# Performance work log

Hardware: AMD Instinct MI355X
Metric: run time of the kernel (lower is better)

## Reference

```python
import jax, jax.numpy as jnp
import numpy as np

N = 50000        # nodes
E = 500000       # edges
NUM = 4          # sampled intermediate neighbors per edge (self.num)
F = 64           # in_feats == out_feats (transform=False)
D = 32           # dist_dim
NB = 64          # embedding rows = len(boundaries)+1


def setup_inputs() -> dict:
    key = jax.random.key(0)
    ks = jax.random.split(key, 10)
    feat = jax.random.normal(ks[0], (N, F), jnp.float32)
    loc = jax.random.uniform(ks[1], (N, 3), jnp.float32)          # 3D positions in unit cube
    boundaries = jnp.sort(jax.random.uniform(ks[2], (NB - 1,), jnp.float32, 0.0, 2.0))
    embed_table = jax.random.normal(ks[3], (NB, D), jnp.float32)
    G_w = jax.random.normal(ks[4], (F, D), jnp.float32) / np.sqrt(D)      # Linear(dist_dim->out, no bias)
    agg_w = jax.random.normal(ks[5], (F, 2 * F), jnp.float32) / np.sqrt(2 * F)  # Linear(2*out->out)
    agg_b = jnp.zeros((F,), jnp.float32)
    src = jax.random.randint(ks[6], (E,), 0, N, jnp.int32)
    dst = jax.random.randint(ks[7], (E,), 0, N, jnp.int32)
    inter_ids = jax.random.randint(ks[8], (E, NUM), 0, N, jnp.int32)
    return dict(feat=feat, loc=loc, boundaries=boundaries, embed_table=embed_table,
                G_w=G_w, agg_w=agg_w, agg_b=agg_b, src=src, dst=dst, inter_ids=inter_ids)


def reference(feat, loc, boundaries, embed_table, G_w, agg_w, agg_b, src, dst, inter_ids):
    n = feat.shape[0]
    ones = jnp.ones((src.shape[0],), feat.dtype)
    # symmetric-ish degree normalization: d0 = in_deg^-0.5, d2 = out_deg^-0.5
    in_deg = jax.ops.segment_sum(ones, dst, num_segments=n)
    out_deg = jax.ops.segment_sum(ones, src, num_segments=n)
    d0 = jnp.clip(in_deg, 1.0) ** -0.5   # [N]
    d2 = jnp.clip(out_deg, 1.0) ** -0.5  # [N]

    # dist1 = ||loc[dst] - loc[src]||_2, bucketize -> embed -> G
    dist1 = jnp.linalg.norm(loc[dst] - loc[src], axis=1)              # [E]
    de1 = embed_table[jnp.searchsorted(boundaries, dist1)] @ G_w.T    # [E, F]

    # intermediate sampled neighbors: dist to each sampled node from edge src
    pos_src = loc[src]                                                # [E, 3]
    inter_pos = loc[inter_ids]                                        # [E, NUM, 3]
    dist_ = jnp.linalg.norm(pos_src[:, None, :] - inter_pos, axis=-1) # [E, NUM]
    de_ = embed_table[jnp.searchsorted(boundaries, dist_)] @ G_w.T    # [E, NUM, F]
    inter_h = feat[inter_ids]                                         # [E, NUM, F]
    dist_embed_dot_h = (de_ * inter_h).mean(axis=1)                   # [E, F]

    # h = d0[dst] * d2[src] * agg_fc([de1 * h_src, dist_embed_dot_h])
    cat = jnp.concatenate([de1 * feat[src], dist_embed_dot_h], axis=1)  # [E, 2F]
    msg = (d0[dst] * d2[src])[:, None] * (cat @ agg_w.T + agg_b)        # [E, F]

    # update_all(copy_e('h'), sum) -> scatter-sum messages to dst
    ft = jax.ops.segment_sum(msg, dst, num_segments=n)                  # [N, F]
    return ft
```

## Files before the change

### kernel.cpp

```cpp
#include <hip/hip_runtime.h>
#include <math.h>

#define LUTN 1024
#define LUTSCALE 512.0f
#define NBINS 50048
#define CHSH 12


__global__ __launch_bounds__(512) void front_kernel(
    const float* __restrict__ embed, const float* __restrict__ G_w,
    const float* __restrict__ boundaries, const float* __restrict__ feat,
    const float* __restrict__ loc,
    const int* __restrict__ src, const int* __restrict__ dst,
    float* __restrict__ M, int* __restrict__ lut,
    unsigned short* __restrict__ featH, float4* __restrict__ loc4,
    unsigned char* __restrict__ pcnt, unsigned char* __restrict__ psrc,
    unsigned char* __restrict__ rnk8,
    int N, int E, int P, int PREPB) {

    __shared__ unsigned int h[NBINS / 4];

    if (blockIdx.x < 2 * P) {
        for (int i = threadIdx.x; i < NBINS / 4; i += 512) h[i] = 0u;
        __syncthreads();

        const int p    = blockIdx.x >> 1;
        const int role = blockIdx.x & 1;
        const int base = p << CHSH;
        const int lim  = min(E - base, 1 << CHSH);

        if (role == 0) {
            for (int t = threadIdx.x; t < lim; t += 512) {
                const int e = base + t;
                const int d = dst[e];
                const unsigned sh = (unsigned)(d & 3) * 8u;
                unsigned old = atomicAdd(&h[d >> 2], 1u << sh);
                rnk8[e] = (unsigned char)((old >> sh) & 0xFFu);
            }
            __syncthreads();
            unsigned int* gc = (unsigned int*)(pcnt + (size_t)p * NBINS);
            for (int i = threadIdx.x; i < NBINS / 4; i += 512) gc[i] = h[i];
        } else {
            for (int t = threadIdx.x; t < lim; t += 512) {
                const int s = src[base + t];
                atomicAdd(&h[s >> 2], 1u << ((unsigned)(s & 3) * 8u));
            }
            __syncthreads();
            unsigned int* gs = (unsigned int*)(psrc + (size_t)p * NBINS);
            for (int i = threadIdx.x; i < NBINS / 4; i += 512) gs[i] = h[i];
        }
        return;
    }

    const int gid = (blockIdx.x - 2 * P) * 512 + threadIdx.x;
    const int gsz = PREPB * 512;
    for (int i = gid; i < 4096; i += gsz) {
        int b = i >> 6, f = i & 63;
        float acc = 0.f;
        #pragma unroll
        for (int dd = 0; dd < 32; ++dd) acc += embed[b * 32 + dd] * G_w[f * 32 + dd];
        M[i] = acc;
    }
    for (int i = gid; i < LUTN; i += gsz) {
        float left = (float)i * (1.0f / LUTSCALE);
        int c = 0;
        for (int j = 0; j < 63; ++j) c += (boundaries[j] < left) ? 1 : 0;
        lut[i] = c;
    }
    const int nq = N * 16;
    for (int i = gid; i < nq; i += gsz) {
        float4 v = ((const float4*)feat)[i];
        unsigned ux = __float_as_uint(v.x), uy = __float_as_uint(v.y);
        unsigned uz = __float_as_uint(v.z), uw = __float_as_uint(v.w);
        ushort4 hh;
        hh.x = (unsigned short)((ux + 0x7FFFu + ((ux >> 16) & 1u)) >> 16);
        hh.y = (unsigned short)((uy + 0x7FFFu + ((uy >> 16) & 1u)) >> 16);
        hh.z = (unsigned short)((uz + 0x7FFFu + ((uz >> 16) & 1u)) >> 16);
        hh.w = (unsigned short)((uw + 0x7FFFu + ((uw >> 16) & 1u)) >> 16);
        ((ushort4*)featH)[i] = hh;
    }
    for (int i = gid; i < N; i += gsz)
        loc4[i] = make_float4(loc[3 * i], loc[3 * i + 1], loc[3 * i + 2], 0.f);
}


__global__ __launch_bounds__(1024) void merge_scan_kernel(
    unsigned char* __restrict__ pcnt, const unsigned char* __restrict__ psrc,
    int* __restrict__ cnt, float* __restrict__ d2w,
    int* __restrict__ startv, int* __restrict__ part, int P, int N) {

    __shared__ int wsum[16];
    const int t = threadIdx.x, lane = t & 63, wv = t >> 6;
    const int d = blockIdx.x * 1024 + t;

    int sc = 0;
    if (d < N) {
        #pragma unroll 4
        for (int p = 0; p < P; ++p) {
            const size_t idx = (size_t)p * NBINS + d;
            const int c = pcnt[idx];
            pcnt[idx] = (unsigned char)sc;
            sc += c;
        }
        cnt[d] = sc;
        int ss = 0;
        #pragma unroll 4
        for (int p = 0; p < P; ++p) ss += psrc[(size_t)p * NBINS + d];
        d2w[d] = rsqrtf(fmaxf((float)ss, 1.0f));
    }

    const int v = sc;
    int x = v;
    #pragma unroll
    for (int off = 1; off < 64; off <<= 1) { int y = __shfl_up(x, off); if (lane >= off) x += y; }
    if (lane == 63) wsum[wv] = x;
    __syncthreads();
    if (t < 16) {
        int w = wsum[t], xx = w;
        #pragma unroll
        for (int off = 1; off < 16; off <<= 1) { int y = __shfl_up(xx, off); if (t >= off) xx += y; }
        wsum[t] = xx - w;
    }
    __syncthreads();
    int incl = x + wsum[wv];
    if (d < N) startv[d] = incl - v;
    if (t == 1023) part[blockIdx.x] = incl;
}

__device__ __forceinline__ void load_chunkoff(const int* __restrict__ part, int nb,
                                              int* __restrict__ co) {
    if (threadIdx.x < 64) {
        int v = (threadIdx.x < nb) ? part[threadIdx.x] : 0;
        int x = v;
        #pragma unroll
        for (int off = 1; off < 64; off <<= 1) {
            int y = __shfl_up(x, off);
            if ((threadIdx.x & 63) >= off) x += y;
        }
        co[threadIdx.x] = x - v;
    }
    __syncthreads();
}


__global__ __launch_bounds__(256) void edge_kernel(
    const float4* __restrict__ loc4, const float* __restrict__ boundaries,
    const int* __restrict__ lut,
    const int* __restrict__ src, const int* __restrict__ dst,
    const int* __restrict__ inter,
    const unsigned char* __restrict__ rnk8, const unsigned char* __restrict__ pcnt,
    const int* __restrict__ startv, const int* __restrict__ part,
    const float* __restrict__ d2w,
    int4* __restrict__ rec, int E, int nb) {

    __shared__ int lut_s[LUTN];
    __shared__ float bl[64];
    __shared__ int co[64];
    ((int4*)lut_s)[threadIdx.x] = ((const int4*)lut)[threadIdx.x];
    if (threadIdx.x < 64)
        bl[threadIdx.x] = (threadIdx.x < 63) ? boundaries[threadIdx.x] : 3.4e38f;
    load_chunkoff(part, nb, co);

    const int ebase = blockIdx.x * 512 + threadIdx.x;

    #pragma unroll
    for (int u = 0; u < 2; ++u) {
        const int e = ebase + u * 256;
        if (e >= E) continue;

        const int s = src[e], d = dst[e];
        const int4 ii = ((const int4*)inter)[e];

        const float4 ps = loc4[s];
        float dist[5];
        {
            float4 pd = loc4[d];
            float dx = pd.x - ps.x, dy = pd.y - ps.y, dz = pd.z - ps.z;
            dist[0] = sqrtf(dx * dx + dy * dy + dz * dz);
        }
        const int id4[4] = {ii.x, ii.y, ii.z, ii.w};
        #pragma unroll
        for (int j = 0; j < 4; ++j) {
            float4 pt = loc4[id4[j]];
            float dx = pt.x - ps.x, dy = pt.y - ps.y, dz = pt.z - ps.z;
            dist[1 + j] = sqrtf(dx * dx + dy * dy + dz * dz);
        }
        unsigned pack = 0;
        #pragma unroll
        for (int q = 0; q < 5; ++q) {
            float dq = dist[q];
            int cell = (int)(dq * LUTSCALE);
            cell = (cell > LUTN - 1) ? (LUTN - 1) : cell;
            int b = lut_s[cell];
            while (b < 63 && bl[b] < dq) ++b;
            while (b > 0 && bl[b - 1] >= dq) --b;
            pack |= ((unsigned)b) << (6 * q);
        }

        const int p = e >> CHSH;
        const int cbase = pcnt[(size_t)p * NBINS + d];
        const int pos = startv[d] + co[d >> 10] + cbase + (int)rnk8[e];
        const float w = d2w[s];
        unsigned uw = __float_as_uint(w);
        unsigned wb = (uw + 0x7FFFu + ((uw >> 16) & 1u)) & 0xFFFF0000u;
        rec[pos] = make_int4(s | (ii.x << 16), ii.y | (ii.z << 16), ii.w | (int)wb, (int)pack);
    }
}


__global__ __launch_bounds__(256) void node_kernel(
    const unsigned short* __restrict__ featH, const float* __restrict__ M,
    const int* __restrict__ cnt, const int* __restrict__ startv,
    const int* __restrict__ part, const int4* __restrict__ rec,
    float* __restrict__ cat, float* __restrict__ swb, int N, int nb) {

    __shared__ float Ms[4096];
    __shared__ int co[64];
    #pragma unroll
    for (int i = 0; i < 4; ++i)
        ((float4*)Ms)[threadIdx.x + 256 * i] = ((const float4*)M)[threadIdx.x + 256 * i];
    load_chunkoff(part, nb, co);

    const int lane = threadIdx.x & 63;
    const int wid  = threadIdx.x >> 6;
    const int d    = blockIdx.x * 4 + wid;
    if (d >= N) return;

    const int deg  = __builtin_amdgcn_readfirstlane(cnt[d]);
    const int base = __builtin_amdgcn_readfirstlane(startv[d] + co[d >> 10]);
    const int4* rp = rec + base;

    float acc0 = 0.f, acc1 = 0.f, sw = 0.f;

    #pragma unroll 4
    for (int k = 0; k < deg; ++k) {
        const int4 r = rp[k];
        const int s  = r.x & 0xFFFF;
        const int i0 = ((unsigned)r.x) >> 16;
        const int i1 = r.y & 0xFFFF;
        const int i2 = ((unsigned)r.y) >> 16;
        const int i3 = r.z & 0xFFFF;
        const float w = __uint_as_float((unsigned)r.z & 0xFFFF0000u);
        const unsigned pk = (unsigned)r.w;

        const float fs = __uint_as_float(((unsigned)featH[(size_t)s  * 64 + lane]) << 16);
        const float f0 = __uint_as_float(((unsigned)featH[(size_t)i0 * 64 + lane]) << 16);
        const float f1 = __uint_as_float(((unsigned)featH[(size_t)i1 * 64 + lane]) << 16);
        const float f2 = __uint_as_float(((unsigned)featH[(size_t)i2 * 64 + lane]) << 16);
        const float f3 = __uint_as_float(((unsigned)featH[(size_t)i3 * 64 + lane]) << 16);
        const float m0 = Ms[(pk & 63u) * 64 + lane];
        const float m1 = Ms[((pk >> 6) & 63u) * 64 + lane];
        const float m2 = Ms[((pk >> 12) & 63u) * 64 + lane];
        const float m3 = Ms[((pk >> 18) & 63u) * 64 + lane];
        const float m4 = Ms[((pk >> 24) & 63u) * 64 + lane];

        acc0 = fmaf(m0 * fs, w, acc0);
        float t = m1 * f0 + m2 * f1 + m3 * f2 + m4 * f3;
        acc1 = fmaf(0.25f * t, w, acc1);
        sw += w;
    }

    cat[(size_t)d * 128 + lane]      = acc0;
    cat[(size_t)d * 128 + 64 + lane] = acc1;
    if (lane == 0) swb[d] = sw;
}


__global__ __launch_bounds__(256) void epilogue_kernel(
    const float* __restrict__ cat, const float* __restrict__ agg_w,
    const float* __restrict__ agg_b, const float* __restrict__ swb,
    const int* __restrict__ cnt, float* __restrict__ out, int N) {

    const int lane = threadIdx.x & 63;
    const int wid  = threadIdx.x >> 6;

    float4 aw[32];
    const float4* awp = (const float4*)(agg_w + (size_t)lane * 128);
    #pragma unroll
    for (int i = 0; i < 32; ++i) aw[i] = awp[i];
    const float bias = agg_b[lane];

    const int gw = blockIdx.x * 4 + wid;
    const int stride = gridDim.x * 4;

    for (int d0i = gw; d0i < N; d0i += stride) {
        const int du = __builtin_amdgcn_readfirstlane(d0i);
        const float* cp = cat + (size_t)du * 128;
        float a0 = bias * swb[du], a1 = 0.f, a2 = 0.f, a3 = 0.f;
        #pragma unroll
        for (int k4 = 0; k4 < 32; k4 += 4) {
            float4 c0 = ((const float4*)cp)[k4];
            float4 c1 = ((const float4*)cp)[k4 + 1];
            float4 c2 = ((const float4*)cp)[k4 + 2];
            float4 c3 = ((const float4*)cp)[k4 + 3];
            a0 = fmaf(aw[k4].x, c0.x, a0); a0 = fmaf(aw[k4].y, c0.y, a0);
            a0 = fmaf(aw[k4].z, c0.z, a0); a0 = fmaf(aw[k4].w, c0.w, a0);
            a1 = fmaf(aw[k4+1].x, c1.x, a1); a1 = fmaf(aw[k4+1].y, c1.y, a1);
            a1 = fmaf(aw[k4+1].z, c1.z, a1); a1 = fmaf(aw[k4+1].w, c1.w, a1);
            a2 = fmaf(aw[k4+2].x, c2.x, a2); a2 = fmaf(aw[k4+2].y, c2.y, a2);
            a2 = fmaf(aw[k4+2].z, c2.z, a2); a2 = fmaf(aw[k4+2].w, c2.w, a2);
            a3 = fmaf(aw[k4+3].x, c3.x, a3); a3 = fmaf(aw[k4+3].y, c3.y, a3);
            a3 = fmaf(aw[k4+3].z, c3.z, a3); a3 = fmaf(aw[k4+3].w, c3.w, a3);
        }
        const float d0v = rsqrtf(fmaxf((float)cnt[du], 1.0f));
        out[(size_t)du * 64 + lane] = d0v * ((a0 + a1) + (a2 + a3));
    }
}


extern "C" void kernel_launch(void* const* d_in, const int* in_sizes, int n_in,
                              void* d_out, int out_size, void* d_ws, size_t ws_size,
                              hipStream_t stream) {
    const float* feat       = (const float*)d_in[0];
    const float* loc        = (const float*)d_in[1];
    const float* boundaries = (const float*)d_in[2];
    const float* embed      = (const float*)d_in[3];
    const float* G_w        = (const float*)d_in[4];
    const float* agg_w      = (const float*)d_in[5];
    const float* agg_b      = (const float*)d_in[6];
    const int*   src        = (const int*)d_in[7];
    const int*   dst        = (const int*)d_in[8];
    const int*   inter      = (const int*)d_in[9];

    const int N = in_sizes[0] / 64;
    const int E = in_sizes[7];

    const int P = (E + (1 << CHSH) - 1) >> CHSH;

    char* w = (char*)d_ws;
    auto take = [&](size_t bytes) { char* p = w; w += (bytes + 15) & ~(size_t)15; return p; };
    float*          M      = (float*)take(4096 * 4);
    int*            lut    = (int*)  take(LUTN * 4);
    int*            cnt    = (int*)  take((size_t)N * 4);
    int*            startv = (int*)  take((size_t)N * 4);
    int*            part   = (int*)  take(64 * 4);
    float*          d2w    = (float*)take((size_t)N * 4);
    int4*           rec    = (int4*) take((size_t)E * 16);
    unsigned char*  rnk8   = (unsigned char*)take((size_t)E);
    unsigned char*  pcnt   = (unsigned char*)take((size_t)P * NBINS);
    unsigned char*  psrc   = (unsigned char*)take((size_t)P * NBINS);
    float*          cat    = (float*)take((size_t)N * 128 * 4);
    float*          swb    = (float*)take((size_t)N * 4);
    unsigned short* featH  = (unsigned short*)take((size_t)N * 64 * 2);
    float4*         loc4   = (float4*)take((size_t)N * 16);
    float*          out    = (float*)d_out;

    const int eb2 = (E + 511) / 512;
    const int nb  = (N + 1023) / 1024;
    const int PREPB = 256;

    front_kernel<<<2 * P + PREPB, 512, 0, stream>>>(embed, G_w, boundaries, feat, loc,
                                                    src, dst, M, lut, featH, loc4,
                                                    pcnt, psrc, rnk8, N, E, P, PREPB);
    merge_scan_kernel<<<nb, 1024, 0, stream>>>(pcnt, psrc, cnt, d2w, startv, part, P, N);
    edge_kernel<<<eb2, 256, 0, stream>>>(loc4, boundaries, lut, src, dst, inter,
                                         rnk8, pcnt, startv, part, d2w, rec, E, nb);
    node_kernel<<<(N + 3) / 4, 256, 0, stream>>>(featH, M, cnt, startv, part, rec,
                                                 cat, swb, N, nb);
    epilogue_kernel<<<768, 256, 0, stream>>>(cat, agg_w, agg_b, swb, cnt, out, N);
}
```

Before: 225.5 us.

## Move per-edge distance bucketing into histogram kernel to overlap with counting

Splits the constant-table and loc4 preparation into a separate small kernel. Per-edge distance computation and bucketization now run in extra blocks of the histogram kernel, concurrently with the degree counting. The later edge kernel becomes a pure scatter that reads a precomputed record and adds the out-degree weight. The aim is to hide the gather-heavy distance work behind the atomic histogram phase. The cost is an extra kernel launch and an additional E×16-byte intermediate write and read.

Result: slower. 237.0 us (+5.1%).

```diff
diff --git a/kernel.cpp b/kernel.cpp
--- a/kernel.cpp
+++ b/kernel.cpp
@@ -7,16 +7,41 @@
 #define CHSH 12
 
 
-__global__ __launch_bounds__(512) void front_kernel(
+__global__ __launch_bounds__(256) void prep0_kernel(
     const float* __restrict__ embed, const float* __restrict__ G_w,
-    const float* __restrict__ boundaries, const float* __restrict__ feat,
-    const float* __restrict__ loc,
+    const float* __restrict__ boundaries, const float* __restrict__ loc,
+    float* __restrict__ M, int* __restrict__ lut,
+    float4* __restrict__ loc4, int N) {
+
+    const int gid = blockIdx.x * 256 + threadIdx.x;
+    const int gsz = gridDim.x * 256;
+    for (int i = gid; i < 4096; i += gsz) {
+        int b = i >> 6, f = i & 63;
+        float acc = 0.f;
+        #pragma unroll
+        for (int dd = 0; dd < 32; ++dd) acc += embed[b * 32 + dd] * G_w[f * 32 + dd];
+        M[i] = acc;
+    }
+    for (int i = gid; i < LUTN; i += gsz) {
+        float left = (float)i * (1.0f / LUTSCALE);
+        int c = 0;
+        for (int j = 0; j < 63; ++j) c += (boundaries[j] < left) ? 1 : 0;
+        lut[i] = c;
+    }
+    for (int i = gid; i < N; i += gsz)
+        loc4[i] = make_float4(loc[3 * i], loc[3 * i + 1], loc[3 * i + 2], 0.f);
+}
+
+
+__global__ __launch_bounds__(512) void front2_kernel(
+    const float* __restrict__ feat, const float4* __restrict__ loc4,
+    const float* __restrict__ boundaries, const int* __restrict__ lut,
     const int* __restrict__ src, const int* __restrict__ dst,
-    float* __restrict__ M, int* __restrict__ lut,
-    unsigned short* __restrict__ featH, float4* __restrict__ loc4,
+    const int* __restrict__ inter,
+    unsigned short* __restrict__ featH,
     unsigned char* __restrict__ pcnt, unsigned char* __restrict__ psrc,
-    unsigned char* __restrict__ rnk8,
-    int N, int E, int P, int PREPB) {
+    unsigned char* __restrict__ rnk8, int4* __restrict__ recE,
+    int N, int E, int P, int GB, int FB) {
 
     __shared__ unsigned int h[NBINS / 4];
 
@@ -52,21 +77,58 @@
         return;
     }
 
-    const int gid = (blockIdx.x - 2 * P) * 512 + threadIdx.x;
-    const int gsz = PREPB * 512;
-    for (int i = gid; i < 4096; i += gsz) {
-        int b = i >> 6, f = i & 63;
-        float acc = 0.f;
-        #pragma unroll
-        for (int dd = 0; dd < 32; ++dd) acc += embed[b * 32 + dd] * G_w[f * 32 + dd];
-        M[i] = acc;
-    }
-    for (int i = gid; i < LUTN; i += gsz) {
-        float left = (float)i * (1.0f / LUTSCALE);
-        int c = 0;
-        for (int j = 0; j < 63; ++j) c += (boundaries[j] < left) ? 1 : 0;
-        lut[i] = c;
-    }
+    if (blockIdx.x < 2 * P + GB) {
+        int*   lut_s = (int*)h;
+        float* bl    = (float*)(h + LUTN);
+        if (threadIdx.x < 256)
+            ((int4*)lut_s)[threadIdx.x] = ((const int4*)lut)[threadIdx.x];
+        else if (threadIdx.x < 320) {
+            const int j = threadIdx.x - 256;
+            bl[j] = (j < 63) ? boundaries[j] : 3.4e38f;
+        }
+        __syncthreads();
+
+        const int ebase = (blockIdx.x - 2 * P) * 1024 + threadIdx.x;
+        #pragma unroll
+        for (int u = 0; u < 2; ++u) {
+            const int e = ebase + u * 512;
+            if (e >= E) continue;
+
+            const int s = src[e], d = dst[e];
+            const int4 ii = ((const int4*)inter)[e];
+
+            const float4 ps = loc4[s];
+            float dist[5];
+            {
+                float4 pd = loc4[d];
+                float dx = pd.x - ps.x, dy = pd.y - ps.y, dz = pd.z - ps.z;
+                dist[0] = sqrtf(dx * dx + dy * dy + dz * dz);
+            }
+            const int id4[4] = {ii.x, ii.y, ii.z, ii.w};
+            #pragma unroll
+            for (int j = 0; j < 4; ++j) {
+                float4 pt = loc4[id4[j]];
+                float dx = pt.x - ps.x, dy = pt.y - ps.y, dz = pt.z - ps.z;
+                dist[1 + j] = sqrtf(dx * dx + dy * dy + dz * dz);
+            }
+            unsigned pack = 0;
+            #pragma unroll
+            for (int q = 0; q < 5; ++q) {
+                float dq = dist[q];
+                int cell = (int)(dq * LUTSCALE);
+                cell = (cell > LUTN - 1) ? (LUTN - 1) : cell;
+                int b = lut_s[cell];
+                while (b < 63 && bl[b] < dq) ++b;
+                while (b > 0 && bl[b - 1] >= dq) --b;
+                pack |= ((unsigned)b) << (6 * q);
+            }
+            recE[e] = make_int4(s | (ii.x << 16), ii.y | (ii.z << 16), ii.w, (int)pack);
+        }
+        return;
+    }
+
+    const int gid = (blockIdx.x - 2 * P - GB) * 512 + threadIdx.x;
+    const int gsz = FB * 512;
     const int nq = N * 16;
     for (int i = gid; i < nq; i += gsz) {
         float4 v = ((const float4*)feat)[i];
@@ -79,8 +141,6 @@
         hh.w = (unsigned short)((uw + 0x7FFFu + ((uw >> 16) & 1u)) >> 16);
         ((ushort4*)featH)[i] = hh;
     }
-    for (int i = gid; i < N; i += gsz)
-        loc4[i] = make_float4(loc[3 * i], loc[3 * i + 1], loc[3 * i + 2], 0.f);
 }
 
 
@@ -143,67 +203,31 @@
 }
 
 
-__global__ __launch_bounds__(256) void edge_kernel(
-    const float4* __restrict__ loc4, const float* __restrict__ boundaries,
-    const int* __restrict__ lut,
-    const int* __restrict__ src, const int* __restrict__ dst,
-    const int* __restrict__ inter,
+__global__ __launch_bounds__(256) void scatter_kernel(
+    const int4* __restrict__ recE, const int* __restrict__ dst,
     const unsigned char* __restrict__ rnk8, const unsigned char* __restrict__ pcnt,
     const int* __restrict__ startv, const int* __restrict__ part,
     const float* __restrict__ d2w,
     int4* __restrict__ rec, int E, int nb) {
 
-    __shared__ int lut_s[LUTN];
-    __shared__ float bl[64];
     __shared__ int co[64];
-    ((int4*)lut_s)[threadIdx.x] = ((const int4*)lut)[threadIdx.x];
-    if (threadIdx.x < 64)
-        bl[threadIdx.x] = (threadIdx.x < 63) ? boundaries[threadIdx.x] : 3.4e38f;
     load_chunkoff(part, nb, co);
 
     const int ebase = blockIdx.x * 512 + threadIdx.x;
-
     #pragma unroll
     for (int u = 0; u < 2; ++u) {
         const int e = ebase + u * 256;
         if (e >= E) continue;
-
-        const int s = src[e], d = dst[e];
-        const int4 ii = ((const int4*)inter)[e];
-
-        const float4 ps = loc4[s];
-        float dist[5];
-        {
-            float4 pd = loc4[d];
-            float dx = pd.x - ps.x, dy = pd.y - ps.y, dz = pd.z - ps.z;
-            dist[0] = sqrtf(dx * dx + dy * dy + dz * dz);
-        }
-        const int id4[4] = {ii.x, ii.y, ii.z, ii.w};
-        #pragma unroll
-        for (int j = 0; j < 4; ++j) {
-            float4 pt = loc4[id4[j]];
-            float dx = pt.x - ps.x, dy = pt.y - ps.y, dz = pt.z - ps.z;
-            dist[1 + j] = sqrtf(dx * dx + dy * dy + dz * dz);
-        }
-        unsigned pack = 0;
-        #pragma unroll
-        for (int q = 0; q < 5; ++q) {
-            float dq = dist[q];
-            int cell = (int)(dq * LUTSCALE);
-            cell = (cell > LUTN - 1) ? (LUTN - 1) : cell;
-            int b = lut_s[cell];
-            while (b < 63 && bl[b] < dq) ++b;
-            while (b > 0 && bl[b - 1] >= dq) --b;
-            pack |= ((unsigned)b) << (6 * q);
-        }
-
+        const int4 a = recE[e];
+        const int s = a.x & 0xFFFF;
+        const int d = dst[e];
         const int p = e >> CHSH;
         const int cbase = pcnt[(size_t)p * NBINS + d];
         const int pos = startv[d] + co[d >> 10] + cbase + (int)rnk8[e];
         const float w = d2w[s];
         unsigned uw = __float_as_uint(w);
         unsigned wb = (uw + 0x7FFFu + ((uw >> 16) & 1u)) & 0xFFFF0000u;
-        rec[pos] = make_int4(s | (ii.x << 16), ii.y | (ii.z << 16), ii.w | (int)wb, (int)pack);
+        rec[pos] = make_int4(a.x, a.y, a.z | (int)wb, a.w);
     }
 }
 
@@ -335,6 +359,7 @@
     int*            startv = (int*)  take((size_t)N * 4);
     int*            part   = (int*)  take(64 * 4);
     float*          d2w    = (float*)take((size_t)N * 4);
+    int4*           recE   = (int4*) take((size_t)E * 16);
     int4*           rec    = (int4*) take((size_t)E * 16);
     unsigned char*  rnk8   = (unsigned char*)take((size_t)E);
     unsigned char*  pcnt   = (unsigned char*)take((size_t)P * NBINS);
@@ -345,16 +370,19 @@
     float4*         loc4   = (float4*)take((size_t)N * 16);
     float*          out    = (float*)d_out;
 
-    const int eb2 = (E + 511) / 512;
     const int nb  = (N + 1023) / 1024;
-    const int PREPB = 256;
-
-    front_kernel<<<2 * P + PREPB, 512, 0, stream>>>(embed, G_w, boundaries, feat, loc,
-                                                    src, dst, M, lut, featH, loc4,
-                                                    pcnt, psrc, rnk8, N, E, P, PREPB);
+    const int GB  = (E + 1023) / 1024;
+    const int FB  = 128;
+    const int sb  = (E + 511) / 512;
+
+    prep0_kernel<<<256, 256, 0, stream>>>(embed, G_w, boundaries, loc, M, lut, loc4, N);
+    front2_kernel<<<2 * P + GB + FB, 512, 0, stream>>>(feat, loc4, boundaries, lut,
+                                                       src, dst, inter, featH,
+                                                       pcnt, psrc, rnk8, recE,
+                                                       N, E, P, GB, FB);
     merge_scan_kernel<<<nb, 1024, 0, stream>>>(pcnt, psrc, cnt, d2w, startv, part, P, N);
-    edge_kernel<<<eb2, 256, 0, stream>>>(loc4, boundaries, lut, src, dst, inter,
-                                         rnk8, pcnt, startv, part, d2w, rec, E, nb);
+    scatter_kernel<<<sb, 256, 0, stream>>>(recE, dst, rnk8, pcnt, startv, part, d2w,
+                                           rec, E, nb);
     node_kernel<<<(N + 3) / 4, 256, 0, stream>>>(featH, M, cnt, startv, part, rec,
                                                  cat, swb, N, nb);
     epilogue_kernel<<<768, 256, 0, stream>>>(cat, agg_w, agg_b, swb, cnt, out, N);
```
